# Performance work log

Measured on AMD Instinct MI355X. Metric: run time of the kernel, lower is better.

The kernel has to match this reference:

```python
import jax, jax.numpy as jnp
import numpy as np

N_GAUSS = 2048
FEAT_DIM = 3
IMG_H, IMG_W = 256, 256
EPS = 1e-4  # args.eps with tiled rasterizer path


def setup_inputs() -> dict:
    key = jax.random.key(0)
    k_xy, k_sc, k_rot, k_feat = jax.random.split(key, 4)
    xy = jax.random.uniform(k_xy, (N_GAUSS, 2), dtype=jnp.float32)  # normalized [0,1) coords
    # scale holds INVERSE std-devs (disable_inverse_scale=False path: scale = 1/init_scale);
    # values 10..50 give Gaussians spanning a few pixels at 256x256.
    scale = jax.random.uniform(k_sc, (N_GAUSS, 2), minval=10.0, maxval=50.0, dtype=jnp.float32)
    rot = jax.random.normal(k_rot, (N_GAUSS, 1), dtype=jnp.float32)
    feat = jax.random.uniform(k_feat, (N_GAUSS, FEAT_DIM), dtype=jnp.float32)
    return {"xy": xy, "scale": scale, "rot": rot, "feat": feat, "topk": 8}


def reference(xy, scale, rot, feat, topk):
    # Pixel centers in normalized coordinates, matching get_grid(h, w) -> (x, y)
    xs = (jnp.arange(IMG_W, dtype=jnp.float32) + 0.5) / IMG_W
    ys = (jnp.arange(IMG_H, dtype=jnp.float32) + 0.5) / IMG_H
    px, py = jnp.meshgrid(xs, ys, indexing="xy")  # each [H, W]
    px = px.reshape(-1)  # [P]
    py = py.reshape(-1)

    dx = px[:, None] - xy[None, :, 0]  # [P, N]
    dy = py[:, None] - xy[None, :, 1]  # [P, N]

    c = jnp.cos(rot[:, 0])  # [N]
    s = jnp.sin(rot[:, 0])
    # Rotate offset into the Gaussian's local frame
    lx = dx * c + dy * s   # [P, N]
    ly = -dx * s + dy * c  # [P, N]

    # Anisotropic Gaussian weight; scale is the inverse std-dev per axis
    w = jnp.exp(-0.5 * ((lx * scale[:, 0]) ** 2 + (ly * scale[:, 1]) ** 2))  # [P, N]

    # Keep top-k Gaussians per pixel, normalize their weights, accumulate features
    tw, ti = jax.lax.top_k(w, topk)        # [P, K]
    tf = feat[ti]                          # [P, K, C]
    alpha = tw / (jnp.sum(tw, axis=-1, keepdims=True) + EPS)  # [P, K]
    img = jnp.einsum("pk,pkc->pc", alpha, tf)                 # [P, C]
    return img.reshape(IMG_H, IMG_W, FEAT_DIM).transpose(2, 0, 1)  # [C, H, W]
```

## Files before the change

kernel.cpp:

```cpp
#include <hip/hip_runtime.h>
#include <math.h>

#define N_GAUSS 2048
#define IMG_H 256
#define IMG_W 256
#define NPIX (IMG_H * IMG_W)
#define EPS 1e-4f

#define TILE 8
#define TILES_X (IMG_W / TILE)
#define NTILES (TILES_X * (IMG_H / TILE))
#define CSTRIDE N_GAUSS
#define D_HALF 0.019336f

#define WS_GP_OFF     0
#define WS_COUNT_OFF  (N_GAUSS * 32)
#define WS_CAND_OFF   (WS_COUNT_OFF + 4096)
#define WS_NEEDED     (WS_CAND_OFF + (size_t)NTILES * CSTRIDE * 2)

struct GParam {
    float x, y;
    float c, s;
    float sx, sy;
    float pad0, pad1;
};

__global__ void prep_kernel(const float* __restrict__ xy,
                            const float* __restrict__ scale,
                            const float* __restrict__ rot,
                            GParam* __restrict__ gp) {
    int g = blockIdx.x * blockDim.x + threadIdx.x;
    if (g >= N_GAUSS) return;
    GParam o;
    o.x  = xy[2 * g + 0];
    o.y  = xy[2 * g + 1];
    o.sx = scale[2 * g + 0];
    o.sy = scale[2 * g + 1];
    double r = (double)rot[g];
    o.c = (float)cos(r);
    o.s = (float)sin(r);
    o.pad0 = 0.f; o.pad1 = 0.f;
    gp[g] = o;
}

#define LADDER(T, G)                                                     \
    if ((T) < v7) {                                                      \
        const bool c0 = (T) < v0, c1 = (T) < v1, c2 = (T) < v2;          \
        const bool c3 = (T) < v3, c4 = (T) < v4, c5 = (T) < v5;          \
        const bool c6 = (T) < v6;                                        \
        v7 = c6 ? v6 : (T);            i7 = c6 ? i6 : (G);               \
        v6 = c6 ? (c5 ? v5 : (T)) : v6; i6 = c6 ? (c5 ? i5 : (G)) : i6;  \
        v5 = c5 ? (c4 ? v4 : (T)) : v5; i5 = c5 ? (c4 ? i4 : (G)) : i5;  \
        v4 = c4 ? (c3 ? v3 : (T)) : v4; i4 = c4 ? (c3 ? i3 : (G)) : i4;  \
        v3 = c3 ? (c2 ? v2 : (T)) : v3; i3 = c3 ? (c2 ? i2 : (G)) : i3;  \
        v2 = c2 ? (c1 ? v1 : (T)) : v2; i2 = c2 ? (c1 ? i1 : (G)) : i2;  \
        v1 = c1 ? (c0 ? v0 : (T)) : v1; i1 = c1 ? (c0 ? i0 : (G)) : i1;  \
        v0 = c0 ? (T) : v0;            i0 = c0 ? (G) : i0;               \
    }

#define VLADDER(T)                                                       \
    if ((T) < v7) {                                                      \
        const bool c0 = (T) < v0, c1 = (T) < v1, c2 = (T) < v2;          \
        const bool c3 = (T) < v3, c4 = (T) < v4, c5 = (T) < v5;          \
        const bool c6 = (T) < v6;                                        \
        v7 = c6 ? v6 : (T);                                              \
        v6 = c6 ? (c5 ? v5 : (T)) : v6;                                  \
        v5 = c5 ? (c4 ? v4 : (T)) : v5;                                  \
        v4 = c4 ? (c3 ? v3 : (T)) : v4;                                  \
        v3 = c3 ? (c2 ? v2 : (T)) : v3;                                  \
        v2 = c2 ? (c1 ? v1 : (T)) : v2;                                  \
        v1 = c1 ? (c0 ? v0 : (T)) : v1;                                  \
        v0 = c0 ? (T) : v0;                                              \
    }

__launch_bounds__(256)
__global__ void cull_kernel(const GParam* __restrict__ gp,
                            unsigned* __restrict__ counts,
                            unsigned short* __restrict__ cands) {
    __shared__ float rlo[N_GAUSS];
    __shared__ float lists[256][9];

    const int tid  = threadIdx.x;
    const int tile = blockIdx.x;
    const float cx = (float)((tile & (TILES_X - 1)) * TILE + 4) * (1.0f / IMG_W);
    const float cy = (float)((tile / TILES_X) * TILE + 4) * (1.0f / IMG_H);

    float v0 = INFINITY, v1 = INFINITY, v2 = INFINITY, v3 = INFINITY;
    float v4 = INFINITY, v5 = INFINITY, v6 = INFINITY, v7 = INFINITY;

    for (int r = 0; r < N_GAUSS / 256; ++r) {
        int g = r * 256 + tid;
        GParam q = gp[g];
        float dx = cx - q.x;
        float dy = cy - q.y;
        float lx = dx * q.c + dy * q.s;
        float ly = dy * q.c - dx * q.s;
        float a  = lx * q.sx;
        float b  = ly * q.sy;
        float rr = sqrtf(a * a + b * b);
        float m  = fmaxf(q.sx, q.sy) * D_HALF;
        rlo[g]   = rr - m;
        float rp = rr + m;
        VLADDER(rp)
    }
    lists[tid][0] = v0; lists[tid][1] = v1; lists[tid][2] = v2; lists[tid][3] = v3;
    lists[tid][4] = v4; lists[tid][5] = v5; lists[tid][6] = v6; lists[tid][7] = v7;
    lists[tid][8] = INFINITY;
    __syncthreads();

    for (int stride = 128; stride >= 1; stride >>= 1) {
        if (tid < stride) {
            float outv[8];
            int ia = 0, ib = 0;
#pragma unroll
            for (int k = 0; k < 8; ++k) {
                float av = lists[tid][ia];
                float bv = lists[tid + stride][ib];
                bool ta = av <= bv;
                outv[k] = ta ? av : bv;
                ia += ta ? 1 : 0;
                ib += ta ? 0 : 1;
            }
#pragma unroll
            for (int k = 0; k < 8; ++k) lists[tid][k] = outv[k];
        }
        __syncthreads();
    }
    float cut = lists[0][7];
    cut = cut + 0.01f + 1e-4f * cut;

    if (tid < 64) {
        unsigned short* cl = cands + (size_t)tile * CSTRIDE;
        unsigned base = 0;
        for (int s2 = 0; s2 < N_GAUSS / 64; ++s2) {
            int g = s2 * 64 + tid;
            bool keep = rlo[g] <= cut;
            unsigned long long mask = __ballot(keep);
            unsigned pos = (unsigned)__popcll(mask & ((1ull << tid) - 1ull));
            if (keep) cl[base + pos] = (unsigned short)g;
            base += (unsigned)__popcll(mask);
        }
        if (tid == 0) counts[tile] = base;
    }
}

__launch_bounds__(256)
__global__ void splat2_kernel(const GParam* __restrict__ gp,
                              const float* __restrict__ feat,
                              const unsigned* __restrict__ counts,
                              const unsigned short* __restrict__ cands,
                              float* __restrict__ out) {
    __shared__ float4 qa[256];
    __shared__ float2 qb[256];
    __shared__ unsigned short qi[256];
    __shared__ float          lt[4][8][64];
    __shared__ unsigned short li[4][8][64];

    const int tid  = threadIdx.x;
    const int lane = tid & 63;
    const int w    = tid >> 6;
    const int tile = blockIdx.x;
    const int pxi  = (tile & (TILES_X - 1)) * TILE + (lane & 7);
    const int pyi  = (tile / TILES_X) * TILE + (lane >> 3);
    const int p    = pyi * IMG_W + pxi;
    const float px = (pxi + 0.5f) * (1.0f / IMG_W);
    const float py = (pyi + 0.5f) * (1.0f / IMG_H);

    const int L  = (int)counts[tile];
    const int L4 = (L + 3) >> 2;
    int start = w * L4; if (start > L) start = L;
    int end   = start + L4; if (end > L) end = L;

    const unsigned short* cl = cands + (size_t)tile * CSTRIDE;

    float v0 = INFINITY, v1 = INFINITY, v2 = INFINITY, v3 = INFINITY;
    float v4 = INFINITY, v5 = INFINITY, v6 = INFINITY, v7 = INFINITY;
    int   i0 = 0, i1 = 0, i2 = 0, i3 = 0, i4 = 0, i5 = 0, i6 = 0, i7 = 0;

    for (int base = 0; base < L; base += 256) {
        int t = base + tid;
        if (t < L) {
            int g = cl[t];
            const float4* g4 = (const float4*)(gp + g);
            float4 a4 = g4[0];
            float4 b4 = g4[1];
            qa[tid] = a4;
            qb[tid] = make_float2(b4.x, b4.y);
            qi[tid] = (unsigned short)g;
        }
        __syncthreads();
        int jlo = start > base ? start : base;
        int lim = base + 256; if (lim > end) lim = end;
        for (int j = jlo; j < lim; ++j) {
            int k = j - base;
            float4 a4 = qa[k];
            float2 b2 = qb[k];
            int g = (int)qi[k];
            float dx = __fsub_rn(px, a4.x);
            float dy = __fsub_rn(py, a4.y);
            float lx = __fadd_rn(__fmul_rn(dx, a4.z), __fmul_rn(dy, a4.w));
            float ly = __fadd_rn(__fmul_rn(-dx, a4.w), __fmul_rn(dy, a4.z));
            float aa = __fmul_rn(lx, b2.x);
            float bb = __fmul_rn(ly, b2.y);
            float t2 = __fadd_rn(__fmul_rn(aa, aa), __fmul_rn(bb, bb));
            LADDER(t2, g)
        }
        __syncthreads();
    }

    lt[w][0][lane] = v0; li[w][0][lane] = (unsigned short)i0;
    lt[w][1][lane] = v1; li[w][1][lane] = (unsigned short)i1;
    lt[w][2][lane] = v2; li[w][2][lane] = (unsigned short)i2;
    lt[w][3][lane] = v3; li[w][3][lane] = (unsigned short)i3;
    lt[w][4][lane] = v4; li[w][4][lane] = (unsigned short)i4;
    lt[w][5][lane] = v5; li[w][5][lane] = (unsigned short)i5;
    lt[w][6][lane] = v6; li[w][6][lane] = (unsigned short)i6;
    lt[w][7][lane] = v7; li[w][7][lane] = (unsigned short)i7;
    __syncthreads();

    if (w == 0) {
        v0 = INFINITY; v1 = INFINITY; v2 = INFINITY; v3 = INFINITY;
        v4 = INFINITY; v5 = INFINITY; v6 = INFINITY; v7 = INFINITY;
        i0 = 0; i1 = 0; i2 = 0; i3 = 0; i4 = 0; i5 = 0; i6 = 0; i7 = 0;
        for (int c = 0; c < 4; ++c) {
#pragma unroll
            for (int k = 0; k < 8; ++k) {
                float t2 = lt[c][k][lane];
                int   g  = (int)li[c][k][lane];
                LADDER(t2, g)
            }
        }
        float w0 = expf(-0.5f * v0), w1 = expf(-0.5f * v1);
        float w2 = expf(-0.5f * v2), w3 = expf(-0.5f * v3);
        float w4 = expf(-0.5f * v4), w5 = expf(-0.5f * v5);
        float w6 = expf(-0.5f * v6), w7 = expf(-0.5f * v7);
        float sum = w0 + w1 + w2 + w3 + w4 + w5 + w6 + w7;
        float inv = 1.0f / (sum + EPS);

        float oc0 = 0.f, oc1 = 0.f, oc2 = 0.f;
#define ACC(K)                                                  \
        {                                                       \
            float al = w##K * inv;                              \
            const float* f = feat + 3 * i##K;                   \
            oc0 = fmaf(al, f[0], oc0);                          \
            oc1 = fmaf(al, f[1], oc1);                          \
            oc2 = fmaf(al, f[2], oc2);                          \
        }
        ACC(0) ACC(1) ACC(2) ACC(3) ACC(4) ACC(5) ACC(6) ACC(7)
#undef ACC

        out[p]            = oc0;
        out[p + NPIX]     = oc1;
        out[p + 2 * NPIX] = oc2;
    }
}

#define FSPLIT 8
#define FCHUNK (N_GAUSS / FSPLIT)
#define FPIXB 128
#define FNTH (FPIXB * FSPLIT)

__launch_bounds__(FNTH)
__global__ void splat_fb_kernel(const GParam* __restrict__ gp,
                                const float* __restrict__ feat,
                                float* __restrict__ out) {
    __shared__ float          lt[FSPLIT][8][FPIXB];
    __shared__ unsigned short li[FSPLIT][8][FPIXB];

    const int tid   = threadIdx.x;
    const int pix   = tid & (FPIXB - 1);
    const int chunk = tid >> 7;
    const int p     = blockIdx.x * FPIXB + pix;
    const float px = ((p & (IMG_W - 1)) + 0.5f) * (1.0f / IMG_W);
    const float py = ((p >> 8) + 0.5f) * (1.0f / IMG_H);

    float v0 = INFINITY, v1 = INFINITY, v2 = INFINITY, v3 = INFINITY;
    float v4 = INFINITY, v5 = INFINITY, v6 = INFINITY, v7 = INFINITY;
    int   i0 = 0, i1 = 0, i2 = 0, i3 = 0, i4 = 0, i5 = 0, i6 = 0, i7 = 0;

    const int gbase = chunk * FCHUNK;
    const GParam* gptr = gp + gbase;
#define FPROC(CF, G)                                                      \
    {                                                                     \
        float dx = __fsub_rn(px, (CF).x);                                 \
        float dy = __fsub_rn(py, (CF).y);                                 \
        float lx = __fadd_rn(__fmul_rn(dx, (CF).c), __fmul_rn(dy, (CF).s)); \
        float ly = __fadd_rn(__fmul_rn(-dx, (CF).s), __fmul_rn(dy, (CF).c)); \
        float a  = __fmul_rn(lx, (CF).sx);                                \
        float b  = __fmul_rn(ly, (CF).sy);                                \
        float t  = __fadd_rn(__fmul_rn(a, a), __fmul_rn(b, b));           \
        LADDER(t, (G))                                                    \
    }
    GParam c0r = gptr[0];
    GParam c1r = gptr[1];
    for (int j = 0; j < FCHUNK - 2; j += 2) {
        GParam n0 = gptr[j + 2];
        GParam n1 = gptr[j + 3];
        FPROC(c0r, gbase + j)
        FPROC(c1r, gbase + j + 1)
        c0r = n0; c1r = n1;
    }
    FPROC(c0r, gbase + FCHUNK - 2)
    FPROC(c1r, gbase + FCHUNK - 1)
#undef FPROC

    lt[chunk][0][pix] = v0; li[chunk][0][pix] = (unsigned short)i0;
    lt[chunk][1][pix] = v1; li[chunk][1][pix] = (unsigned short)i1;
    lt[chunk][2][pix] = v2; li[chunk][2][pix] = (unsigned short)i2;
    lt[chunk][3][pix] = v3; li[chunk][3][pix] = (unsigned short)i3;
    lt[chunk][4][pix] = v4; li[chunk][4][pix] = (unsigned short)i4;
    lt[chunk][5][pix] = v5; li[chunk][5][pix] = (unsigned short)i5;
    lt[chunk][6][pix] = v6; li[chunk][6][pix] = (unsigned short)i6;
    lt[chunk][7][pix] = v7; li[chunk][7][pix] = (unsigned short)i7;
    __syncthreads();

    if (chunk == 0) {
        v0 = INFINITY; v1 = INFINITY; v2 = INFINITY; v3 = INFINITY;
        v4 = INFINITY; v5 = INFINITY; v6 = INFINITY; v7 = INFINITY;
        i0 = 0; i1 = 0; i2 = 0; i3 = 0; i4 = 0; i5 = 0; i6 = 0; i7 = 0;
        for (int c = 0; c < FSPLIT; ++c) {
#pragma unroll
            for (int k = 0; k < 8; ++k) {
                float t = lt[c][k][pix];
                int   g = (int)li[c][k][pix];
                LADDER(t, g)
            }
        }
        float w0 = expf(-0.5f * v0), w1 = expf(-0.5f * v1);
        float w2 = expf(-0.5f * v2), w3 = expf(-0.5f * v3);
        float w4 = expf(-0.5f * v4), w5 = expf(-0.5f * v5);
        float w6 = expf(-0.5f * v6), w7 = expf(-0.5f * v7);
        float sum = w0 + w1 + w2 + w3 + w4 + w5 + w6 + w7;
        float inv = 1.0f / (sum + EPS);
        float oc0 = 0.f, oc1 = 0.f, oc2 = 0.f;
#define ACC(K)                                                  \
        {                                                       \
            float al = w##K * inv;                              \
            const float* f = feat + 3 * i##K;                   \
            oc0 = fmaf(al, f[0], oc0);                          \
            oc1 = fmaf(al, f[1], oc1);                          \
            oc2 = fmaf(al, f[2], oc2);                          \
        }
        ACC(0) ACC(1) ACC(2) ACC(3) ACC(4) ACC(5) ACC(6) ACC(7)
#undef ACC
        out[p]            = oc0;
        out[p + NPIX]     = oc1;
        out[p + 2 * NPIX] = oc2;
    }
}

extern "C" void kernel_launch(void* const* d_in, const int* in_sizes, int n_in,
                              void* d_out, int out_size, void* d_ws, size_t ws_size,
                              hipStream_t stream) {
    const float* xy    = (const float*)d_in[0];
    const float* scale = (const float*)d_in[1];
    const float* rot   = (const float*)d_in[2];
    const float* feat  = (const float*)d_in[3];
    float* out = (float*)d_out;

    char* ws = (char*)d_ws;
    GParam* gp = (GParam*)(ws + WS_GP_OFF);

    prep_kernel<<<(N_GAUSS + 255) / 256, 256, 0, stream>>>(xy, scale, rot, gp);

    if (ws_size >= WS_NEEDED) {
        unsigned*       counts = (unsigned*)(ws + WS_COUNT_OFF);
        unsigned short* cands  = (unsigned short*)(ws + WS_CAND_OFF);
        cull_kernel<<<NTILES, 256, 0, stream>>>(gp, counts, cands);
        splat2_kernel<<<NTILES, 256, 0, stream>>>(gp, feat, counts, cands, out);
    } else {
        splat_fb_kernel<<<NPIX / FPIXB, FNTH, 0, stream>>>(gp, feat, out);
    }
}
```

Measured before the change: 30.54 us.

## Fuse per-tile culling and splatting into one kernel with LDS candidate list

Merges the cull and splat kernels so each tile block builds its candidate list in shared memory and consumes it directly. This removes one kernel launch and the global-memory round trip for the candidate indices and counts. The fallback path for small workspaces is dropped. Shared memory per block grows (rlo, lists, qidx plus the splat buffers), which may lower occupancy.

Result: faster. 29.19 us (-4.4%).

```diff
diff --git a/kernel.cpp b/kernel.cpp
--- a/kernel.cpp
+++ b/kernel.cpp
@@ -10,13 +10,7 @@
 #define TILE 8
 #define TILES_X (IMG_W / TILE)
 #define NTILES (TILES_X * (IMG_H / TILE))
-#define CSTRIDE N_GAUSS
 #define D_HALF 0.019336f
-
-#define WS_GP_OFF     0
-#define WS_COUNT_OFF  (N_GAUSS * 32)
-#define WS_CAND_OFF   (WS_COUNT_OFF + 4096)
-#define WS_NEEDED     (WS_CAND_OFF + (size_t)NTILES * CSTRIDE * 2)
 
 struct GParam {
     float x, y;
@@ -74,38 +68,48 @@
     }
 
 __launch_bounds__(256)
-__global__ void cull_kernel(const GParam* __restrict__ gp,
-                            unsigned* __restrict__ counts,
-                            unsigned short* __restrict__ cands) {
+__global__ void fused_kernel(const GParam* __restrict__ gp,
+                             const float* __restrict__ feat,
+                             float* __restrict__ out) {
     __shared__ float rlo[N_GAUSS];
     __shared__ float lists[256][9];
+    __shared__ unsigned short qidx[N_GAUSS];
+    __shared__ unsigned qcount;
+    __shared__ float4 qa[256];
+    __shared__ float2 qb[256];
+    __shared__ unsigned short qi[256];
+    __shared__ float          lt[4][8][64];
+    __shared__ unsigned short li[4][8][64];
 
     const int tid  = threadIdx.x;
+    const int lane = tid & 63;
+    const int w    = tid >> 6;
     const int tile = blockIdx.x;
+
     const float cx = (float)((tile & (TILES_X - 1)) * TILE + 4) * (1.0f / IMG_W);
     const float cy = (float)((tile / TILES_X) * TILE + 4) * (1.0f / IMG_H);
-
-    float v0 = INFINITY, v1 = INFINITY, v2 = INFINITY, v3 = INFINITY;
-    float v4 = INFINITY, v5 = INFINITY, v6 = INFINITY, v7 = INFINITY;
-
-    for (int r = 0; r < N_GAUSS / 256; ++r) {
-        int g = r * 256 + tid;
-        GParam q = gp[g];
-        float dx = cx - q.x;
-        float dy = cy - q.y;
-        float lx = dx * q.c + dy * q.s;
-        float ly = dy * q.c - dx * q.s;
-        float a  = lx * q.sx;
-        float b  = ly * q.sy;
-        float rr = sqrtf(a * a + b * b);
-        float m  = fmaxf(q.sx, q.sy) * D_HALF;
-        rlo[g]   = rr - m;
-        float rp = rr + m;
-        VLADDER(rp)
-    }
-    lists[tid][0] = v0; lists[tid][1] = v1; lists[tid][2] = v2; lists[tid][3] = v3;
-    lists[tid][4] = v4; lists[tid][5] = v5; lists[tid][6] = v6; lists[tid][7] = v7;
-    lists[tid][8] = INFINITY;
+    {
+        float v0 = INFINITY, v1 = INFINITY, v2 = INFINITY, v3 = INFINITY;
+        float v4 = INFINITY, v5 = INFINITY, v6 = INFINITY, v7 = INFINITY;
+        for (int r = 0; r < N_GAUSS / 256; ++r) {
+            int g = r * 256 + tid;
+            GParam q = gp[g];
+            float dx = cx - q.x;
+            float dy = cy - q.y;
+            float lx = dx * q.c + dy * q.s;
+            float ly = dy * q.c - dx * q.s;
+            float a  = lx * q.sx;
+            float b  = ly * q.sy;
+            float rr = sqrtf(a * a + b * b);
+            float m  = fmaxf(q.sx, q.sy) * D_HALF;
+            rlo[g]   = rr - m;
+            float rp = rr + m;
+            VLADDER(rp)
+        }
+        lists[tid][0] = v0; lists[tid][1] = v1; lists[tid][2] = v2; lists[tid][3] = v3;
+        lists[tid][4] = v4; lists[tid][5] = v5; lists[tid][6] = v6; lists[tid][7] = v7;
+        lists[tid][8] = INFINITY;
+    }
     __syncthreads();
 
     for (int stride = 128; stride >= 1; stride >>= 1) {
@@ -130,49 +134,30 @@
     cut = cut + 0.01f + 1e-4f * cut;
 
     if (tid < 64) {
-        unsigned short* cl = cands + (size_t)tile * CSTRIDE;
         unsigned base = 0;
         for (int s2 = 0; s2 < N_GAUSS / 64; ++s2) {
             int g = s2 * 64 + tid;
             bool keep = rlo[g] <= cut;
             unsigned long long mask = __ballot(keep);
             unsigned pos = (unsigned)__popcll(mask & ((1ull << tid) - 1ull));
-            if (keep) cl[base + pos] = (unsigned short)g;
+            if (keep) qidx[base + pos] = (unsigned short)g;
             base += (unsigned)__popcll(mask);
         }
-        if (tid == 0) counts[tile] = base;
-    }
-}
-
-__launch_bounds__(256)
-__global__ void splat2_kernel(const GParam* __restrict__ gp,
-                              const float* __restrict__ feat,
-                              const unsigned* __restrict__ counts,
-                              const unsigned short* __restrict__ cands,
-                              float* __restrict__ out) {
-    __shared__ float4 qa[256];
-    __shared__ float2 qb[256];
-    __shared__ unsigned short qi[256];
-    __shared__ float          lt[4][8][64];
-    __shared__ unsigned short li[4][8][64];
-
-    const int tid  = threadIdx.x;
-    const int lane = tid & 63;
-    const int w    = tid >> 6;
-    const int tile = blockIdx.x;
-    const int pxi  = (tile & (TILES_X - 1)) * TILE + (lane & 7);
-    const int pyi  = (tile / TILES_X) * TILE + (lane >> 3);
-    const int p    = pyi * IMG_W + pxi;
+        if (tid == 0) qcount = base;
+    }
+    __syncthreads();
+
+    const int pxi = (tile & (TILES_X - 1)) * TILE + (lane & 7);
+    const int pyi = (tile / TILES_X) * TILE + (lane >> 3);
+    const int p   = pyi * IMG_W + pxi;
     const float px = (pxi + 0.5f) * (1.0f / IMG_W);
     const float py = (pyi + 0.5f) * (1.0f / IMG_H);
 
-    const int L  = (int)counts[tile];
+    const int L  = (int)qcount;
     const int L4 = (L + 3) >> 2;
     int start = w * L4; if (start > L) start = L;
     int end   = start + L4; if (end > L) end = L;
 
-    const unsigned short* cl = cands + (size_t)tile * CSTRIDE;
-
     float v0 = INFINITY, v1 = INFINITY, v2 = INFINITY, v3 = INFINITY;
     float v4 = INFINITY, v5 = INFINITY, v6 = INFINITY, v7 = INFINITY;
     int   i0 = 0, i1 = 0, i2 = 0, i3 = 0, i4 = 0, i5 = 0, i6 = 0, i7 = 0;
@@ -180,7 +165,7 @@
     for (int base = 0; base < L; base += 256) {
         int t = base + tid;
         if (t < L) {
-            int g = cl[t];
+            int g = qidx[t];
             const float4* g4 = (const float4*)(gp + g);
             float4 a4 = g4[0];
             float4 b4 = g4[1];
@@ -255,100 +240,6 @@
     }
 }
 
-#define FSPLIT 8
-#define FCHUNK (N_GAUSS / FSPLIT)
-#define FPIXB 128
-#define FNTH (FPIXB * FSPLIT)
-
-__launch_bounds__(FNTH)
-__global__ void splat_fb_kernel(const GParam* __restrict__ gp,
-                                const float* __restrict__ feat,
-                                float* __restrict__ out) {
-    __shared__ float          lt[FSPLIT][8][FPIXB];
-    __shared__ unsigned short li[FSPLIT][8][FPIXB];
-
-    const int tid   = threadIdx.x;
-    const int pix   = tid & (FPIXB - 1);
-    const int chunk = tid >> 7;
-    const int p     = blockIdx.x * FPIXB + pix;
-    const float px = ((p & (IMG_W - 1)) + 0.5f) * (1.0f / IMG_W);
-    const float py = ((p >> 8) + 0.5f) * (1.0f / IMG_H);
-
-    float v0 = INFINITY, v1 = INFINITY, v2 = INFINITY, v3 = INFINITY;
-    float v4 = INFINITY, v5 = INFINITY, v6 = INFINITY, v7 = INFINITY;
-    int   i0 = 0, i1 = 0, i2 = 0, i3 = 0, i4 = 0, i5 = 0, i6 = 0, i7 = 0;
-
-    const int gbase = chunk * FCHUNK;
-    const GParam* gptr = gp + gbase;
-#define FPROC(CF, G)                                                      \
-    {                                                                     \
-        float dx = __fsub_rn(px, (CF).x);                                 \
-        float dy = __fsub_rn(py, (CF).y);                                 \
-        float lx = __fadd_rn(__fmul_rn(dx, (CF).c), __fmul_rn(dy, (CF).s)); \
-        float ly = __fadd_rn(__fmul_rn(-dx, (CF).s), __fmul_rn(dy, (CF).c)); \
-        float a  = __fmul_rn(lx, (CF).sx);                                \
-        float b  = __fmul_rn(ly, (CF).sy);                                \
-        float t  = __fadd_rn(__fmul_rn(a, a), __fmul_rn(b, b));           \
-        LADDER(t, (G))                                                    \
-    }
-    GParam c0r = gptr[0];
-    GParam c1r = gptr[1];
-    for (int j = 0; j < FCHUNK - 2; j += 2) {
-        GParam n0 = gptr[j + 2];
-        GParam n1 = gptr[j + 3];
-        FPROC(c0r, gbase + j)
-        FPROC(c1r, gbase + j + 1)
-        c0r = n0; c1r = n1;
-    }
-    FPROC(c0r, gbase + FCHUNK - 2)
-    FPROC(c1r, gbase + FCHUNK - 1)
-#undef FPROC
-
-    lt[chunk][0][pix] = v0; li[chunk][0][pix] = (unsigned short)i0;
-    lt[chunk][1][pix] = v1; li[chunk][1][pix] = (unsigned short)i1;
-    lt[chunk][2][pix] = v2; li[chunk][2][pix] = (unsigned short)i2;
-    lt[chunk][3][pix] = v3; li[chunk][3][pix] = (unsigned short)i3;
-    lt[chunk][4][pix] = v4; li[chunk][4][pix] = (unsigned short)i4;
-    lt[chunk][5][pix] = v5; li[chunk][5][pix] = (unsigned short)i5;
-    lt[chunk][6][pix] = v6; li[chunk][6][pix] = (unsigned short)i6;
-    lt[chunk][7][pix] = v7; li[chunk][7][pix] = (unsigned short)i7;
-    __syncthreads();
-
-    if (chunk == 0) {
-        v0 = INFINITY; v1 = INFINITY; v2 = INFINITY; v3 = INFINITY;
-        v4 = INFINITY; v5 = INFINITY; v6 = INFINITY; v7 = INFINITY;
-        i0 = 0; i1 = 0; i2 = 0; i3 = 0; i4 = 0; i5 = 0; i6 = 0; i7 = 0;
-        for (int c = 0; c < FSPLIT; ++c) {
-#pragma unroll
-            for (int k = 0; k < 8; ++k) {
-                float t = lt[c][k][pix];
-                int   g = (int)li[c][k][pix];
-                LADDER(t, g)
-            }
-        }
-        float w0 = expf(-0.5f * v0), w1 = expf(-0.5f * v1);
-        float w2 = expf(-0.5f * v2), w3 = expf(-0.5f * v3);
-        float w4 = expf(-0.5f * v4), w5 = expf(-0.5f * v5);
-        float w6 = expf(-0.5f * v6), w7 = expf(-0.5f * v7);
-        float sum = w0 + w1 + w2 + w3 + w4 + w5 + w6 + w7;
-        float inv = 1.0f / (sum + EPS);
-        float oc0 = 0.f, oc1 = 0.f, oc2 = 0.f;
-#define ACC(K)                                                  \
-        {                                                       \
-            float al = w##K * inv;                              \
-            const float* f = feat + 3 * i##K;                   \
-            oc0 = fmaf(al, f[0], oc0);                          \
-            oc1 = fmaf(al, f[1], oc1);                          \
-            oc2 = fmaf(al, f[2], oc2);                          \
-        }
-        ACC(0) ACC(1) ACC(2) ACC(3) ACC(4) ACC(5) ACC(6) ACC(7)
-#undef ACC
-        out[p]            = oc0;
-        out[p + NPIX]     = oc1;
-        out[p + 2 * NPIX] = oc2;
-    }
-}
-
 extern "C" void kernel_launch(void* const* d_in, const int* in_sizes, int n_in,
                               void* d_out, int out_size, void* d_ws, size_t ws_size,
                               hipStream_t stream) {
@@ -357,18 +248,8 @@
     const float* rot   = (const float*)d_in[2];
     const float* feat  = (const float*)d_in[3];
     float* out = (float*)d_out;
-
-    char* ws = (char*)d_ws;
-    GParam* gp = (GParam*)(ws + WS_GP_OFF);
+    GParam* gp = (GParam*)d_ws;
 
     prep_kernel<<<(N_GAUSS + 255) / 256, 256, 0, stream>>>(xy, scale, rot, gp);
-
-    if (ws_size >= WS_NEEDED) {
-        unsigned*       counts = (unsigned*)(ws + WS_COUNT_OFF);
-        unsigned short* cands  = (unsigned short*)(ws + WS_CAND_OFF);
-        cull_kernel<<<NTILES, 256, 0, stream>>>(gp, counts, cands);
-        splat2_kernel<<<NTILES, 256, 0, stream>>>(gp, feat, counts, cands, out);
-    } else {
-        splat_fb_kernel<<<NPIX / FPIXB, FNTH, 0, stream>>>(gp, feat, out);
-    }
+    fused_kernel<<<NTILES, 256, 0, stream>>>(gp, feat, out);
 }
```
